# Optimization experiments

Measured on AMD Instinct MI355X. Metric: run time of the kernel, lower is better.

The kernel has to match this reference:

```python
import jax, jax.numpy as jnp
import numpy as np

B, N, M, C = 8, 2048, 2048, 3


def setup_inputs() -> dict:
    key = jax.random.key(0)
    k1, k2, k3 = jax.random.split(key, 3)
    source = jax.random.normal(k1, (B, N, C), dtype=jnp.float32)
    target = jax.random.normal(k2, (B, M, C), dtype=jnp.float32)
    # binary float mask over target points (1 = valid)
    mask = (jax.random.uniform(k3, (B, M)) > 0.5).astype(jnp.float32)
    return {"source": source, "target": target, "mask": mask}


def reference(source, target, mask):
    # criterion_mode='l1': per-coordinate |diff|, summed over C
    # diff: [B, N, M, C] -> distance: [B, N, M]
    distance = jnp.abs(source[:, :, None, :] - target[:, None, :, :]).sum(-1)
    # max over whole tensor, detached
    max_dist = jax.lax.stop_gradient(distance.max())
    # subtract max_dist where mask==1 so min over dst only picks masked (valid) points
    new_distance = distance - mask[:, None, :] * max_dist  # [B, N, M]
    src2dst = new_distance.min(axis=2) + max_dist          # [B, N]
    dst2src = distance.min(axis=1)                         # [B, M]
    # src_weight = dst_weight = 1.0, dynamic_weight = False
    # reduction='mean'
    loss_src = jnp.mean(src2dst)
    loss_dst = (dst2src * mask).sum() / mask.sum()
    # loss_src_weight = loss_dst_weight = 1.0; return_indices=False
    return (loss_src, loss_dst)
```

## Files before the change

### kernel.cpp

```cpp
#include <hip/hip_runtime.h>

#define BB 8
#define NN 2048
#define MM 2048
#define TS 128
#define NT_M (MM / TS)
#define NT_N (NN / TS)

struct Accums { float ssum, dsum, msum; unsigned cnt; };

__global__ __launch_bounds__(256) void dist_kernel(const float* __restrict__ src,
                                                   const float* __restrict__ tgt,
                                                   const float* __restrict__ mask,
                                                   float* __restrict__ spart,
                                                   float* __restrict__ dpart,
                                                   Accums* __restrict__ acc) {
    __shared__ float4 ss[TS];
    __shared__ float4 st[TS];
    __shared__ float pA[8][TS];
    __shared__ float pB[8][TS];

    const int b  = blockIdx.z;
    const int n0 = blockIdx.y * TS;
    const int m0 = blockIdx.x * TS;
    const int t  = threadIdx.x;
    const float INF = __int_as_float(0x7F800000);

    if (blockIdx.x == 0 && blockIdx.y == 0 && blockIdx.z == 0 && t == 0) {
        acc->ssum = 0.f; acc->dsum = 0.f; acc->msum = 0.f; acc->cnt = 0u;
    }

    if (t < TS) {
        const float* sp = src + ((size_t)b * NN + n0 + t) * 3;
        ss[t] = make_float4(sp[0], sp[1], sp[2], 0.f);
    } else {
        const int j = t - TS;
        const float* tp = tgt + ((size_t)b * MM + m0 + j) * 3;
        const float mk = mask[(size_t)b * MM + m0 + j];
        st[j] = make_float4(tp[0], tp[1], tp[2], (mk != 0.f) ? 0.f : INF);
    }
    __syncthreads();

    const int o = t & 31;
    const int g = t >> 5;

    {
        const float4 a0 = ss[o], a1 = ss[o + 32], a2 = ss[o + 64], a3 = ss[o + 96];
        float m0_ = INF, m1_ = INF, m2_ = INF, m3_ = INF;
#pragma unroll
        for (int jj = 0; jj < 16; ++jj) {
            const float4 w = st[g * 16 + jj];
            m0_ = fminf(m0_, fabsf(a0.x - w.x) + fabsf(a0.y - w.y) + fabsf(a0.z - w.z) + w.w);
            m1_ = fminf(m1_, fabsf(a1.x - w.x) + fabsf(a1.y - w.y) + fabsf(a1.z - w.z) + w.w);
            m2_ = fminf(m2_, fabsf(a2.x - w.x) + fabsf(a2.y - w.y) + fabsf(a2.z - w.z) + w.w);
            m3_ = fminf(m3_, fabsf(a3.x - w.x) + fabsf(a3.y - w.y) + fabsf(a3.z - w.z) + w.w);
        }
        pA[g][o] = m0_; pA[g][o + 32] = m1_; pA[g][o + 64] = m2_; pA[g][o + 96] = m3_;
    }

    {
        const float4 b0 = st[o], b1 = st[o + 32], b2 = st[o + 64], b3 = st[o + 96];
        float m0_ = INF, m1_ = INF, m2_ = INF, m3_ = INF;
#pragma unroll
        for (int jj = 0; jj < 16; ++jj) {
            const float4 w = ss[g * 16 + jj];
            m0_ = fminf(m0_, fabsf(b0.x - w.x) + fabsf(b0.y - w.y) + fabsf(b0.z - w.z));
            m1_ = fminf(m1_, fabsf(b1.x - w.x) + fabsf(b1.y - w.y) + fabsf(b1.z - w.z));
            m2_ = fminf(m2_, fabsf(b2.x - w.x) + fabsf(b2.y - w.y) + fabsf(b2.z - w.z));
            m3_ = fminf(m3_, fabsf(b3.x - w.x) + fabsf(b3.y - w.y) + fabsf(b3.z - w.z));
        }
        pB[g][o] = m0_; pB[g][o + 32] = m1_; pB[g][o + 64] = m2_; pB[g][o + 96] = m3_;
    }

    __syncthreads();

    if (t < TS) {
        float mn = pA[0][t];
#pragma unroll
        for (int k = 1; k < 8; ++k) mn = fminf(mn, pA[k][t]);
        spart[((size_t)(b * NT_M + blockIdx.x)) * NN + n0 + t] = mn;
    } else {
        const int p = t - TS;
        float mn = pB[0][p];
#pragma unroll
        for (int k = 1; k < 8; ++k) mn = fminf(mn, pB[k][p]);
        dpart[((size_t)(b * NT_N + blockIdx.y)) * MM + m0 + p] = mn;
    }
}

__global__ __launch_bounds__(256) void reduce_kernel(const float* __restrict__ spart,
                                                     const float* __restrict__ dpart,
                                                     const float* __restrict__ mask,
                                                     Accums* __restrict__ acc,
                                                     float* __restrict__ out) {
    const int t   = threadIdx.x;
    const int idx = blockIdx.x * 256 + t;
    const int b   = idx >> 11;
    const int q   = idx & (NN - 1);

    const float INF = __int_as_float(0x7F800000);
    float smin = INF, dmin = INF;
#pragma unroll
    for (int k = 0; k < NT_M; ++k)
        smin = fminf(smin, spart[((size_t)(b * NT_M + k)) * NN + q]);
#pragma unroll
    for (int k = 0; k < NT_N; ++k)
        dmin = fminf(dmin, dpart[((size_t)(b * NT_N + k)) * MM + q]);

    const float mk = mask[(size_t)b * MM + q];
    float vs = smin, vd = dmin * mk, vm = mk;

    for (int off = 32; off; off >>= 1) {
        vs += __shfl_down(vs, off);
        vd += __shfl_down(vd, off);
        vm += __shfl_down(vm, off);
    }

    __shared__ float w0[4], w1[4], w2[4];
    const int lane = t & 63, wid = t >> 6;
    if (lane == 0) { w0[wid] = vs; w1[wid] = vd; w2[wid] = vm; }
    __syncthreads();

    if (t == 0) {
        float a = 0.f, c = 0.f, d = 0.f;
        for (int i = 0; i < 4; ++i) { a += w0[i]; c += w1[i]; d += w2[i]; }
        atomicAdd(&acc->ssum, a);
        atomicAdd(&acc->dsum, c);
        atomicAdd(&acc->msum, d);
        __threadfence();
        const unsigned old = atomicAdd(&acc->cnt, 1u);
        if (old == gridDim.x - 1) {
            const float S  = atomicAdd(&acc->ssum, 0.f);
            const float D  = atomicAdd(&acc->dsum, 0.f);
            const float Mm = atomicAdd(&acc->msum, 0.f);
            out[0] = S / (float)(BB * NN);
            out[1] = D / Mm;
        }
    }
}

extern "C" void kernel_launch(void* const* d_in, const int* in_sizes, int n_in,
                              void* d_out, int out_size, void* d_ws, size_t ws_size,
                              hipStream_t stream) {
    const float* src  = (const float*)d_in[0];
    const float* tgt  = (const float*)d_in[1];
    const float* mask = (const float*)d_in[2];
    float* out = (float*)d_out;

    float*  spart = (float*)d_ws;
    float*  dpart = spart + (size_t)BB * NT_M * NN;
    Accums* acc   = (Accums*)(dpart + (size_t)BB * NT_N * MM);

    dim3 grid(NT_M, NT_N, BB);
    dist_kernel<<<grid, 256, 0, stream>>>(src, tgt, mask, spart, dpart, acc);
    reduce_kernel<<<64, 256, 0, stream>>>(spart, dpart, mask, acc, out);
}
```

Before: 71.69 us.

## Fuse partial-min reduction into distance kernel via atomicMin and last-block finish

Drops the per-tile partial buffers and the separate reduction kernel. Each block now merges its row and column minima into global per-point arrays with unsigned atomicMin, which orders non-negative floats correctly. The buffers and a ticket counter are set to 0xFF by a memset, so the block that draws ticket NBLK-2 is the last one and computes both final means. This removes a kernel launch and the partial-buffer round trip through memory. The cost is atomic contention, an extra memset, and a serial single-block final reduction over 32K values.

Result: slower. 214.1 us (+198.6%).

```diff
diff --git a/kernel.cpp b/kernel.cpp
--- a/kernel.cpp
+++ b/kernel.cpp
@@ -6,29 +6,27 @@
 #define TS 128
 #define NT_M (MM / TS)
 #define NT_N (NN / TS)
+#define NBLK (NT_M * NT_N * BB)
 
-struct Accums { float ssum, dsum, msum; unsigned cnt; };
 
 __global__ __launch_bounds__(256) void dist_kernel(const float* __restrict__ src,
                                                    const float* __restrict__ tgt,
                                                    const float* __restrict__ mask,
-                                                   float* __restrict__ spart,
-                                                   float* __restrict__ dpart,
-                                                   Accums* __restrict__ acc) {
+                                                   unsigned* __restrict__ smin,
+                                                   unsigned* __restrict__ dmin,
+                                                   unsigned* __restrict__ cnt,
+                                                   float* __restrict__ out) {
     __shared__ float4 ss[TS];
     __shared__ float4 st[TS];
     __shared__ float pA[8][TS];
     __shared__ float pB[8][TS];
+    __shared__ unsigned ticket;
 
     const int b  = blockIdx.z;
     const int n0 = blockIdx.y * TS;
     const int m0 = blockIdx.x * TS;
     const int t  = threadIdx.x;
     const float INF = __int_as_float(0x7F800000);
-
-    if (blockIdx.x == 0 && blockIdx.y == 0 && blockIdx.z == 0 && t == 0) {
-        acc->ssum = 0.f; acc->dsum = 0.f; acc->msum = 0.f; acc->cnt = 0u;
-    }
 
     if (t < TS) {
         const float* sp = src + ((size_t)b * NN + n0 + t) * 3;
@@ -78,37 +76,32 @@
         float mn = pA[0][t];
 #pragma unroll
         for (int k = 1; k < 8; ++k) mn = fminf(mn, pA[k][t]);
-        spart[((size_t)(b * NT_M + blockIdx.x)) * NN + n0 + t] = mn;
+        atomicMin(&smin[(size_t)b * NN + n0 + t], __float_as_uint(mn));
     } else {
         const int p = t - TS;
         float mn = pB[0][p];
 #pragma unroll
         for (int k = 1; k < 8; ++k) mn = fminf(mn, pB[k][p]);
-        dpart[((size_t)(b * NT_N + blockIdx.y)) * MM + m0 + p] = mn;
+        atomicMin(&dmin[(size_t)b * MM + m0 + p], __float_as_uint(mn));
     }
-}
 
-__global__ __launch_bounds__(256) void reduce_kernel(const float* __restrict__ spart,
-                                                     const float* __restrict__ dpart,
-                                                     const float* __restrict__ mask,
-                                                     Accums* __restrict__ acc,
-                                                     float* __restrict__ out) {
-    const int t   = threadIdx.x;
-    const int idx = blockIdx.x * 256 + t;
-    const int b   = idx >> 11;
-    const int q   = idx & (NN - 1);
+    __threadfence();
+    __syncthreads();
+    if (t == 0) ticket = atomicAdd(cnt, 1u);
+    __syncthreads();
+    if (ticket != (unsigned)(NBLK - 2)) return;
 
-    const float INF = __int_as_float(0x7F800000);
-    float smin = INF, dmin = INF;
-#pragma unroll
-    for (int k = 0; k < NT_M; ++k)
-        smin = fminf(smin, spart[((size_t)(b * NT_M + k)) * NN + q]);
-#pragma unroll
-    for (int k = 0; k < NT_N; ++k)
-        dmin = fminf(dmin, dpart[((size_t)(b * NT_N + k)) * MM + q]);
-
-    const float mk = mask[(size_t)b * MM + q];
-    float vs = smin, vd = dmin * mk, vm = mk;
+    float vs = 0.f, vd = 0.f, vm = 0.f;
+    for (int i = t; i < BB * NN; i += 256) {
+        unsigned u = __hip_atomic_load(&smin[i], __ATOMIC_RELAXED, __HIP_MEMORY_SCOPE_AGENT);
+        vs += __uint_as_float(u);
+    }
+    for (int i = t; i < BB * MM; i += 256) {
+        const float mk = mask[i];
+        unsigned u = __hip_atomic_load(&dmin[i], __ATOMIC_RELAXED, __HIP_MEMORY_SCOPE_AGENT);
+        vd += __uint_as_float(u) * mk;
+        vm += mk;
+    }
 
     for (int off = 32; off; off >>= 1) {
         vs += __shfl_down(vs, off);
@@ -124,18 +117,8 @@
     if (t == 0) {
         float a = 0.f, c = 0.f, d = 0.f;
         for (int i = 0; i < 4; ++i) { a += w0[i]; c += w1[i]; d += w2[i]; }
-        atomicAdd(&acc->ssum, a);
-        atomicAdd(&acc->dsum, c);
-        atomicAdd(&acc->msum, d);
-        __threadfence();
-        const unsigned old = atomicAdd(&acc->cnt, 1u);
-        if (old == gridDim.x - 1) {
-            const float S  = atomicAdd(&acc->ssum, 0.f);
-            const float D  = atomicAdd(&acc->dsum, 0.f);
-            const float Mm = atomicAdd(&acc->msum, 0.f);
-            out[0] = S / (float)(BB * NN);
-            out[1] = D / Mm;
-        }
+        out[0] = a / (float)(BB * NN);
+        out[1] = c / d;
     }
 }
 
@@ -147,11 +130,13 @@
     const float* mask = (const float*)d_in[2];
     float* out = (float*)d_out;
 
-    float*  spart = (float*)d_ws;
-    float*  dpart = spart + (size_t)BB * NT_M * NN;
-    Accums* acc   = (Accums*)(dpart + (size_t)BB * NT_N * MM);
+    unsigned* smin = (unsigned*)d_ws;
+    unsigned* dmin = smin + (size_t)BB * NN;
+    unsigned* cnt  = dmin + (size_t)BB * MM;
+
+    const size_t init_bytes = ((size_t)BB * NN + (size_t)BB * MM + 1) * sizeof(unsigned);
+    hipMemsetAsync(d_ws, 0xFF, init_bytes, stream);
 
     dim3 grid(NT_M, NT_N, BB);
-    dist_kernel<<<grid, 256, 0, stream>>>(src, tgt, mask, spart, dpart, acc);
-    reduce_kernel<<<64, 256, 0, stream>>>(spart, dpart, mask, acc, out);
+    dist_kernel<<<grid, 256, 0, stream>>>(src, tgt, mask, smin, dmin, cnt, out);
 }
```
